# Optimization experiments

Measured on AMD Instinct MI355X. Metric: run time of the kernel, lower is better.

The kernel has to match this reference:

```python
import jax, jax.numpy as jnp
import numpy as np

EPS = 1e-6      # delta in ixaxaar/pytorch-dnc util.py and Memory.reset
CLIP = 20.0     # DNC default controller-output clip
M, Wc, R, H, IN, OUT = 10, 20, 1, 256, 27, 128
NN_IN = IN + R * Wc                 # 47 controller input size
IFACE = R * Wc + 3 * Wc + 5 * R + 3  # 88 interface vector size


def _cosine_weights(mem, keys, strengths):
    # mem (B,M,Wc), keys (B,K,Wc), strengths (B,K) -> softmax over cells of scaled cosine sim
    mem_n = mem / (jnp.linalg.norm(mem, axis=2, keepdims=True) + EPS)
    key_n = keys / (jnp.linalg.norm(keys, axis=2, keepdims=True) + EPS)
    d = jnp.einsum('bkw,bmw->bkm', key_n, mem_n)
    return jax.nn.softmax(d * strengths[:, :, None], axis=2)


def _dnc_classifier(x, W_ih, W_hh, b_ih, b_hh, W_xi, b_xi, W_fc, b_fc):
    B, T, _ = x.shape
    # ixaxaar's dnc.py builds inputs[t] = cat(x_t, last_read) ONCE with the initial
    # (zero) last_read, so read vectors never feed the next-step input.
    pad = jnp.zeros((B, R * Wc), x.dtype)
    eye_mask = 1.0 - jnp.eye(M, dtype=x.dtype)

    def step(state, x_t):
        h, c, mem, link, prec, rw, ww, usage = state
        # ---- LSTM controller (1 hidden layer, torch gate order i,f,g,o) ----
        inp = jnp.concatenate([x_t, pad], axis=1)                 # (B,47)
        gates = inp @ W_ih.T + b_ih + h @ W_hh.T + b_hh           # (B,4H)
        i, f, g, o = jnp.split(gates, 4, axis=1)
        c = jax.nn.sigmoid(f) * c + jax.nn.sigmoid(i) * jnp.tanh(g)
        h = jax.nn.sigmoid(o) * jnp.tanh(c)
        out = jnp.clip(h, -CLIP, CLIP)
        # ---- interface vector ----
        xi = out @ W_xi.T + b_xi                                  # (B,88)
        p = R * Wc
        rk = jnp.tanh(xi[:, :p]).reshape(B, R, Wc)                # read keys
        rs = jax.nn.softplus(xi[:, p:p + R]); p += R              # read strengths
        wk = jnp.tanh(xi[:, p:p + Wc]).reshape(B, 1, Wc); p += Wc # write key
        ws = jax.nn.softplus(xi[:, p:p + 1]); p += 1              # write strength
        ev = jax.nn.sigmoid(xi[:, p:p + Wc]); p += Wc             # erase vector
        wv = jnp.tanh(xi[:, p:p + Wc]); p += Wc                   # write vector
        fg = jax.nn.sigmoid(xi[:, p:p + R]); p += R               # free gates
        ag = jax.nn.sigmoid(xi[:, p:p + 1]); p += 1               # allocation gate
        wg = jax.nn.sigmoid(xi[:, p:p + 1]); p += 1               # write gate
        rm = jax.nn.softmax(xi[:, p:p + 3 * R].reshape(B, R, 3), axis=-1)  # read modes (b,f,c)
        # ---- usage (uses PREVIOUS write/read weights) ----
        usage = usage + (1 - usage) * ww
        usage = usage * jnp.prod(1 - fg[:, :, None] * rw, axis=1)
        # ---- write weighting: content + allocation (sort-based free list) ----
        cw = _cosine_weights(mem, wk, ws)[:, 0]                   # (B,M)
        u2 = EPS + (1 - EPS) * usage
        phi = jnp.argsort(u2, axis=1)
        su = jnp.take_along_axis(u2, phi, axis=1)
        prod_excl = jnp.cumprod(jnp.concatenate([jnp.ones((B, 1), u2.dtype), su], axis=1), axis=1)[:, :-1]
        alloc = jnp.take_along_axis((1 - su) * prod_excl, jnp.argsort(phi, axis=1), axis=1)
        ww = wg * (ag * alloc + (1 - ag) * cw)                    # (B,M)
        # ---- erase + write memory ----
        mem = mem * (1 - ww[:, :, None] * ev[:, None, :]) + ww[:, :, None] * wv[:, None, :]
        # ---- temporal link matrix + precedence ----
        link = (1 - ww[:, :, None] - ww[:, None, :]) * link + ww[:, :, None] * prec[:, None, :]
        link = link * eye_mask
        prec = (1 - jnp.sum(ww, axis=1, keepdims=True)) * prec + ww
        # ---- read weighting (content + forward/backward temporal) ----
        cwr = _cosine_weights(mem, rk, rs)                        # (B,R,M)
        fw = jnp.einsum('brm,bnm->brn', rw, link)                 # forward  = L @ w
        bw = jnp.einsum('brm,bmn->brn', rw, link)                 # backward = L^T @ w
        rw = rm[:, :, 0:1] * bw + rm[:, :, 1:2] * fw + rm[:, :, 2:3] * cwr
        return (h, c, mem, link, prec, rw, ww, usage), None

    z = jnp.zeros
    state0 = (z((B, H), x.dtype), z((B, H), x.dtype),
              jnp.full((B, M, Wc), EPS, x.dtype), z((B, M, M), x.dtype),
              z((B, M), x.dtype), jnp.full((B, R, M), EPS, x.dtype),
              jnp.full((B, M), EPS, x.dtype), z((B, M), x.dtype))
    (h, *_), _ = jax.lax.scan(step, state0, jnp.swapaxes(x, 0, 1))
    # classifier head: fc1 on final controller hidden state
    return h @ W_fc.T + b_fc


def setup_inputs() -> dict:
    key = jax.random.key(0)
    ks = jax.random.split(key, 10)
    B, T = 128, 512
    kb = 1.0 / np.sqrt(H)
    u = lambda kk, shape: jax.random.uniform(kk, shape, jnp.float32, -kb, kb)
    return {
        'x': jax.random.normal(ks[0], (B, T, IN), jnp.float32),
        'input_lengths': jax.random.randint(ks[1], (B,), 1, T + 1).astype(jnp.int32),
        'W_ih': u(ks[2], (4 * H, NN_IN)),
        'W_hh': u(ks[3], (4 * H, H)),
        'b_ih': u(ks[4], (4 * H,)),
        'b_hh': u(ks[5], (4 * H,)),
        'W_xi': u(ks[6], (IFACE, H)),
        'b_xi': u(ks[7], (IFACE,)),
        'W_fc': u(ks[8], (OUT, H)),
        'b_fc': u(ks[9], (OUT,)),
    }


def reference(x, input_lengths, W_ih, W_hh, b_ih, b_hh, W_xi, b_xi, W_fc, b_fc):
    # input_lengths is unpacked and discarded by DNCClassifier.forward
    return _dnc_classifier(x, W_ih, W_hh, b_ih, b_hh, W_xi, b_xi, W_fc, b_fc)
```

## Files before the change

kernel.cpp:

```cpp
#include <hip/hip_runtime.h>
#include <hip/hip_fp16.h>


typedef _Float16 h2t __attribute__((ext_vector_type(2)));
typedef unsigned int u32x4 __attribute__((ext_vector_type(4)));

#if defined(__has_builtin)
#  if __has_builtin(__builtin_amdgcn_fdot2)
#    define HAVE_FDOT2 1
#  endif
#endif

__device__ __forceinline__ h2t bc2(unsigned int v) {
  union { unsigned int u; h2t h; } x; x.u = v; return x.h;
}
__device__ __forceinline__ unsigned int pk(float a, float b) {
  union { h2t h; unsigned int u; } x;
  x.h[0] = (_Float16)a; x.h[1] = (_Float16)b;
  return x.u;
}
__device__ __forceinline__ float fdot2f(h2t a, h2t b, float c) {
#ifdef HAVE_FDOT2
  return __builtin_amdgcn_fdot2(a, b, c, false);
#else
  return c + (float)a[0] * (float)b[0] + (float)a[1] * (float)b[1];
#endif
}
__device__ __forceinline__ float dot4(u32x4 w, u32x4 h, float a) {
  a = fdot2f(bc2(w[0]), bc2(h[0]), a);
  a = fdot2f(bc2(w[1]), bc2(h[1]), a);
  a = fdot2f(bc2(w[2]), bc2(h[2]), a);
  a = fdot2f(bc2(w[3]), bc2(h[3]), a);
  return a;
}
__device__ __forceinline__ float sigmf_(float x) {
  return 1.f / (1.f + __expf(-x));
}
__device__ __forceinline__ float tanhf_(float x) {
  float xc = fminf(15.f, fmaxf(-15.f, x));
  float e = __expf(2.f * xc);
  return (e - 1.f) / (e + 1.f);
}
__device__ __forceinline__ float dpp_x1(float x) {
  return __int_as_float(
      __builtin_amdgcn_mov_dpp(__float_as_int(x), 0xB1, 0xF, 0xF, true));
}
__device__ __forceinline__ float dpp_x2(float x) {
  return __int_as_float(
      __builtin_amdgcn_mov_dpp(__float_as_int(x), 0x4E, 0xF, 0xF, true));
}

#define WS_P_OFF      0ull
#define WS_WSCAN_OFF  134217728ull
#define WS_WLDS_OFF   134643712ull
#define WS_WSTR_OFF   134725632ull
#define WS_NEED       134742016ull

__global__ void prep_w(const float* __restrict__ W_hh,
                       unsigned char* __restrict__ ws) {
  int idx = blockIdx.x * 256 + threadIdx.x;
  unsigned int* dst; int j, f;
  if (idx < 106496) {
    j = idx; dst = (unsigned int*)(ws + WS_WSCAN_OFF); f = (j >> 2) >> 9;
  } else if (idx < 126976) {
    j = idx - 106496; dst = (unsigned int*)(ws + WS_WLDS_OFF);
    f = 52 + ((j >> 2) >> 9);
  } else {
    j = idx - 126976; dst = (unsigned int*)(ws + WS_WSTR_OFF);
    f = 62 + ((j >> 2) >> 9);
  }
  int e = j & 3, vv = (j >> 2) & 511;
  int w = vv >> 6, l = vv & 63, kq = l & 3, p = l >> 2;
  int q = f >> 3, uu = (f >> 2) & 1, g = f & 3;
  int u = w * 32 + 2 * p + uu;
  int row = g * 256 + u;
  int k2 = kq * 32 + q * 4 + e;
  dst[j] = pk(W_hh[row * 256 + 2 * k2], W_hh[row * 256 + 2 * k2 + 1]);
}

__global__ __launch_bounds__(256) void prep_p(const float* __restrict__ x,
                                              const float* __restrict__ W_ih,
                                              const float* __restrict__ b_ih,
                                              const float* __restrict__ b_hh,
                                              unsigned char* __restrict__ ws) {
  __shared__ unsigned int sX[64][14];
  const int u = threadIdx.x;
  const int t = blockIdx.x >> 1;
  const int b0 = (blockIdx.x & 1) << 6;
  unsigned int wih[4][14];
  float bias[4];
#pragma unroll
  for (int g = 0; g < 4; ++g) {
    const float* row = W_ih + (size_t)(g * 256 + u) * 47;
    bias[g] = b_ih[g * 256 + u] + b_hh[g * 256 + u];
#pragma unroll
    for (int j = 0; j < 14; ++j) {
      float a = row[2 * j];
      float b = (2 * j + 1 < 27) ? row[2 * j + 1] : 0.f;
      wih[g][j] = pk(a, b);
    }
  }
#pragma unroll 1
  for (int j = u; j < 896; j += 256) {
    int row = j / 14, c2 = j - 14 * row;
    const float* xr = x + ((size_t)(b0 + row) * 512 + t) * 27;
    float a = xr[2 * c2];
    float bb = (2 * c2 + 1 < 27) ? xr[2 * c2 + 1] : 0.f;
    sX[row][c2] = pk(a, bb);
  }
  __syncthreads();
  uint2* Pout = (uint2*)(ws + WS_P_OFF);
#pragma unroll 2
  for (int p = 0; p < 64; ++p) {
    float a0 = bias[0], a1 = bias[1], a2 = bias[2], a3 = bias[3];
#pragma unroll
    for (int j = 0; j < 14; ++j) {
      h2t xx = bc2(sX[p][j]);
      a0 = fdot2f(bc2(wih[0][j]), xx, a0);
      a1 = fdot2f(bc2(wih[1][j]), xx, a1);
      a2 = fdot2f(bc2(wih[2][j]), xx, a2);
      a3 = fdot2f(bc2(wih[3][j]), xx, a3);
    }
    uint2 o; o.x = pk(a0, a1); o.y = pk(a2, a3);
    Pout[((size_t)t * 128 + (b0 + p)) * 256 + u] = o;
  }
}

__global__ __launch_bounds__(512, 2) void scan_k(
    const unsigned char* __restrict__ ws, const float* __restrict__ W_fc,
    const float* __restrict__ b_fc, float* __restrict__ out) {
  __shared__ u32x4 sWq[10 * 512];
  __shared__ __align__(16) unsigned int sH[2][160];
  __shared__ float sHF[256];
  const int v = threadIdx.x;
  const int b = blockIdx.x;
  const int l = v & 63;
  const int w = v >> 6;
  const int kq = l & 3;
  const int p = l >> 2;
  const int u_own = w * 32 + 2 * p + ((l >> 1) & 1);

  u32x4 wr[52];
  {
    const u32x4* wsc = (const u32x4*)(ws + WS_WSCAN_OFF);
#pragma unroll
    for (int f = 0; f < 52; ++f) wr[f] = wsc[f * 512 + v];
  }
  {
    const u32x4* wld = (const u32x4*)(ws + WS_WLDS_OFF);
#pragma unroll
    for (int fl = 0; fl < 10; ++fl) sWq[fl * 512 + v] = wld[fl * 512 + v];
  }
  const u32x4* wstr = (const u32x4*)(ws + WS_WSTR_OFF);

  if (v < 320) ((unsigned int*)sH)[v] = 0u;
  const uint2* Pbuf = (const uint2*)(ws + WS_P_OFF);
  const char* hbase = (const char*)sH;
  char* hwbase = (char*)sH;
  const int kqoff = kq * 144;
  float c = 0.f, hval = 0.f;
  __syncthreads();

#pragma unroll 1
  for (int t = 0; t < 512; ++t) {
    u32x4 tw0 = wstr[0 * 512 + v];
    u32x4 tw1 = wstr[1 * 512 + v];
    uint2 pP = Pbuf[((size_t)t * 128 + b) * 256 + u_own];

    const char* hb = hbase + (t & 1) * 640 + kqoff;
    float aA0 = 0.f, aA1 = 0.f, aA2 = 0.f, aA3 = 0.f;
    float aB0 = 0.f, aB1 = 0.f, aB2 = 0.f, aB3 = 0.f;
    u32x4 hq;
    hq = *(const u32x4*)(hb + 0);
    aA0 = dot4(wr[0], hq, aA0);  aA1 = dot4(wr[1], hq, aA1);
    aA2 = dot4(wr[2], hq, aA2);  aA3 = dot4(wr[3], hq, aA3);
    aB0 = dot4(wr[4], hq, aB0);  aB1 = dot4(wr[5], hq, aB1);
    aB2 = dot4(wr[6], hq, aB2);  aB3 = dot4(wr[7], hq, aB3);
    hq = *(const u32x4*)(hb + 16);
    aA0 = dot4(wr[8], hq, aA0);  aA1 = dot4(wr[9], hq, aA1);
    aA2 = dot4(wr[10], hq, aA2); aA3 = dot4(wr[11], hq, aA3);
    aB0 = dot4(wr[12], hq, aB0); aB1 = dot4(wr[13], hq, aB1);
    aB2 = dot4(wr[14], hq, aB2); aB3 = dot4(wr[15], hq, aB3);
    hq = *(const u32x4*)(hb + 32);
    aA0 = dot4(wr[16], hq, aA0); aA1 = dot4(wr[17], hq, aA1);
    aA2 = dot4(wr[18], hq, aA2); aA3 = dot4(wr[19], hq, aA3);
    aB0 = dot4(wr[20], hq, aB0); aB1 = dot4(wr[21], hq, aB1);
    aB2 = dot4(wr[22], hq, aB2); aB3 = dot4(wr[23], hq, aB3);
    hq = *(const u32x4*)(hb + 48);
    aA0 = dot4(wr[24], hq, aA0); aA1 = dot4(wr[25], hq, aA1);
    aA2 = dot4(wr[26], hq, aA2); aA3 = dot4(wr[27], hq, aA3);
    aB0 = dot4(wr[28], hq, aB0); aB1 = dot4(wr[29], hq, aB1);
    aB2 = dot4(wr[30], hq, aB2); aB3 = dot4(wr[31], hq, aB3);
    hq = *(const u32x4*)(hb + 64);
    aA0 = dot4(wr[32], hq, aA0); aA1 = dot4(wr[33], hq, aA1);
    aA2 = dot4(wr[34], hq, aA2); aA3 = dot4(wr[35], hq, aA3);
    aB0 = dot4(wr[36], hq, aB0); aB1 = dot4(wr[37], hq, aB1);
    aB2 = dot4(wr[38], hq, aB2); aB3 = dot4(wr[39], hq, aB3);
    hq = *(const u32x4*)(hb + 80);
    aA0 = dot4(wr[40], hq, aA0); aA1 = dot4(wr[41], hq, aA1);
    aA2 = dot4(wr[42], hq, aA2); aA3 = dot4(wr[43], hq, aA3);
    aB0 = dot4(wr[44], hq, aB0); aB1 = dot4(wr[45], hq, aB1);
    aB2 = dot4(wr[46], hq, aB2); aB3 = dot4(wr[47], hq, aB3);
    hq = *(const u32x4*)(hb + 96);
    aA0 = dot4(wr[48], hq, aA0); aA1 = dot4(wr[49], hq, aA1);
    aA2 = dot4(wr[50], hq, aA2); aA3 = dot4(wr[51], hq, aA3);
    aB0 = dot4(sWq[0 * 512 + v], hq, aB0); aB1 = dot4(sWq[1 * 512 + v], hq, aB1);
    aB2 = dot4(sWq[2 * 512 + v], hq, aB2); aB3 = dot4(sWq[3 * 512 + v], hq, aB3);
    hq = *(const u32x4*)(hb + 112);
    aA0 = dot4(sWq[4 * 512 + v], hq, aA0); aA1 = dot4(sWq[5 * 512 + v], hq, aA1);
    aA2 = dot4(sWq[6 * 512 + v], hq, aA2); aA3 = dot4(sWq[7 * 512 + v], hq, aA3);
    aB0 = dot4(sWq[8 * 512 + v], hq, aB0); aB1 = dot4(sWq[9 * 512 + v], hq, aB1);
    aB2 = dot4(tw0, hq, aB2); aB3 = dot4(tw1, hq, aB3);

    aA0 += dpp_x1(aA0); aA0 += dpp_x2(aA0);
    aA1 += dpp_x1(aA1); aA1 += dpp_x2(aA1);
    aA2 += dpp_x1(aA2); aA2 += dpp_x2(aA2);
    aA3 += dpp_x1(aA3); aA3 += dpp_x2(aA3);
    aB0 += dpp_x1(aB0); aB0 += dpp_x2(aB0);
    aB1 += dpp_x1(aB1); aB1 += dpp_x2(aB1);
    aB2 += dpp_x1(aB2); aB2 += dpp_x2(aB2);
    aB3 += dpp_x1(aB3); aB3 += dpp_x2(aB3);

    float gi = (l & 2) ? aB0 : aA0;
    float gf = (l & 2) ? aB1 : aA1;
    float gg = (l & 2) ? aB2 : aA2;
    float go = (l & 2) ? aB3 : aA3;
    h2t p01 = bc2(pP.x), p23 = bc2(pP.y);
    gi += (float)p01[0]; gf += (float)p01[1];
    gg += (float)p23[0]; go += (float)p23[1];
    c = sigmf_(gf) * c + sigmf_(gi) * tanhf_(gg);
    hval = sigmf_(go) * tanhf_(c);
    if (!(l & 1)) {
      _Float16* hw = (_Float16*)(hwbase + ((t + 1) & 1) * 640);
      hw[u_own + (u_own >> 6) * 8] = (_Float16)hval;
    }
    __syncthreads();
  }

  if (!(l & 1)) sHF[u_own] = hval;
  __syncthreads();
  if (v < 128) {
    const float4* wrow = (const float4*)(W_fc + (size_t)v * 256);
    float a = b_fc[v];
#pragma unroll 8
    for (int q = 0; q < 64; ++q) {
      float4 wq = wrow[q];
      float4 hh = ((const float4*)sHF)[q];
      a += wq.x * hh.x + wq.y * hh.y + wq.z * hh.z + wq.w * hh.w;
    }
    out[(size_t)b * 128 + v] = a;
  }
}

extern "C" void kernel_launch(void* const* d_in, const int* in_sizes, int n_in,
                              void* d_out, int out_size, void* d_ws,
                              size_t ws_size, hipStream_t stream) {
  const float* x    = (const float*)d_in[0];
  const float* W_ih = (const float*)d_in[2];
  const float* W_hh = (const float*)d_in[3];
  const float* b_ih = (const float*)d_in[4];
  const float* b_hh = (const float*)d_in[5];
  const float* W_fc = (const float*)d_in[8];
  const float* b_fc = (const float*)d_in[9];
  unsigned char* ws = (unsigned char*)d_ws;

  if (ws_size < WS_NEED) return;

  prep_w<<<512, 256, 0, stream>>>(W_hh, ws);
  prep_p<<<1024, 256, 0, stream>>>(x, W_ih, b_ih, b_hh, ws);
  scan_k<<<128, 512, 0, stream>>>(ws, W_fc, b_fc, (float*)d_out);
}
```

Baseline: 917.9 us.

## Double scan block to 1024 threads, one hidden unit per 4-lane group

Reorganizes the recurrent scan so each 1024-thread block gives every hidden unit its own 4-lane group computing all four gates, instead of 512 threads each doing two units' worth of gate dot products. Per-thread register weights drop from 52 to 24 vectors, and the remaining 8 slices go to LDS, which removes the per-step global weight stream loads. The aim is to halve the serial per-step dot-product chain and the select logic. In exchange, each block-wide barrier now synchronizes 16 waves, and only one block of 1024 threads can fit per CU.

```diff
diff --git a/kernel.cpp b/kernel.cpp
--- a/kernel.cpp
+++ b/kernel.cpp
@@ -50,32 +50,22 @@
       __builtin_amdgcn_mov_dpp(__float_as_int(x), 0x4E, 0xF, 0xF, true));
 }
 
-#define WS_P_OFF      0ull
-#define WS_WSCAN_OFF  134217728ull
-#define WS_WLDS_OFF   134643712ull
-#define WS_WSTR_OFF   134725632ull
-#define WS_NEED       134742016ull
+#define WS_P_OFF   0ull
+#define WS_W_OFF   134217728ull
+#define WS_NEED    134742016ull
 
 __global__ void prep_w(const float* __restrict__ W_hh,
                        unsigned char* __restrict__ ws) {
   int idx = blockIdx.x * 256 + threadIdx.x;
-  unsigned int* dst; int j, f;
-  if (idx < 106496) {
-    j = idx; dst = (unsigned int*)(ws + WS_WSCAN_OFF); f = (j >> 2) >> 9;
-  } else if (idx < 126976) {
-    j = idx - 106496; dst = (unsigned int*)(ws + WS_WLDS_OFF);
-    f = 52 + ((j >> 2) >> 9);
-  } else {
-    j = idx - 126976; dst = (unsigned int*)(ws + WS_WSTR_OFF);
-    f = 62 + ((j >> 2) >> 9);
-  }
-  int e = j & 3, vv = (j >> 2) & 511;
-  int w = vv >> 6, l = vv & 63, kq = l & 3, p = l >> 2;
-  int q = f >> 3, uu = (f >> 2) & 1, g = f & 3;
-  int u = w * 32 + 2 * p + uu;
+  int f = idx >> 12, rem = idx & 4095;
+  int v = rem >> 2, e = rem & 3;
+  int w = v >> 6, l = v & 63, kq = l & 3, pl = l >> 2;
+  int u = w * 16 + pl;
+  int j = f >> 2, g = f & 3;
   int row = g * 256 + u;
-  int k2 = kq * 32 + q * 4 + e;
-  dst[j] = pk(W_hh[row * 256 + 2 * k2], W_hh[row * 256 + 2 * k2 + 1]);
+  int k2 = kq * 32 + j * 4 + e;
+  ((unsigned int*)(ws + WS_W_OFF))[idx] =
+      pk(W_hh[row * 256 + 2 * k2], W_hh[row * 256 + 2 * k2 + 1]);
 }
 
 __global__ __launch_bounds__(256) void prep_p(const float* __restrict__ x,
@@ -126,10 +116,10 @@
   }
 }
 
-__global__ __launch_bounds__(512, 2) void scan_k(
+__global__ __launch_bounds__(1024) void scan_k(
     const unsigned char* __restrict__ ws, const float* __restrict__ W_fc,
     const float* __restrict__ b_fc, float* __restrict__ out) {
-  __shared__ u32x4 sWq[10 * 512];
+  __shared__ u32x4 sWq[8 * 1024];
   __shared__ __align__(16) unsigned int sH[2][160];
   __shared__ float sHF[256];
   const int v = threadIdx.x;
@@ -137,107 +127,79 @@
   const int l = v & 63;
   const int w = v >> 6;
   const int kq = l & 3;
-  const int p = l >> 2;
-  const int u_own = w * 32 + 2 * p + ((l >> 1) & 1);
-
-  u32x4 wr[52];
-  {
-    const u32x4* wsc = (const u32x4*)(ws + WS_WSCAN_OFF);
-#pragma unroll
-    for (int f = 0; f < 52; ++f) wr[f] = wsc[f * 512 + v];
-  }
-  {
-    const u32x4* wld = (const u32x4*)(ws + WS_WLDS_OFF);
-#pragma unroll
-    for (int fl = 0; fl < 10; ++fl) sWq[fl * 512 + v] = wld[fl * 512 + v];
-  }
-  const u32x4* wstr = (const u32x4*)(ws + WS_WSTR_OFF);
+  const int pl = l >> 2;
+  const int u = w * 16 + pl;
+
+  const u32x4* Wall = (const u32x4*)(ws + WS_W_OFF);
+  u32x4 wr[24];
+#pragma unroll
+  for (int f = 0; f < 24; ++f) wr[f] = Wall[f * 1024 + v];
+#pragma unroll
+  for (int f = 0; f < 8; ++f) sWq[f * 1024 + v] = Wall[(24 + f) * 1024 + v];
 
   if (v < 320) ((unsigned int*)sH)[v] = 0u;
   const uint2* Pbuf = (const uint2*)(ws + WS_P_OFF);
   const char* hbase = (const char*)sH;
-  char* hwbase = (char*)sH;
   const int kqoff = kq * 144;
+  const int hwb = (u >> 6) * 144 + ((u & 63) >> 1) * 4 + (u & 1) * 2;
   float c = 0.f, hval = 0.f;
   __syncthreads();
 
 #pragma unroll 1
   for (int t = 0; t < 512; ++t) {
-    u32x4 tw0 = wstr[0 * 512 + v];
-    u32x4 tw1 = wstr[1 * 512 + v];
-    uint2 pP = Pbuf[((size_t)t * 128 + b) * 256 + u_own];
+    uint2 pP = Pbuf[((size_t)t * 128 + b) * 256 + u];
 
     const char* hb = hbase + (t & 1) * 640 + kqoff;
-    float aA0 = 0.f, aA1 = 0.f, aA2 = 0.f, aA3 = 0.f;
-    float aB0 = 0.f, aB1 = 0.f, aB2 = 0.f, aB3 = 0.f;
+    float a0 = 0.f, a1 = 0.f, a2 = 0.f, a3 = 0.f;
     u32x4 hq;
     hq = *(const u32x4*)(hb + 0);
-    aA0 = dot4(wr[0], hq, aA0);  aA1 = dot4(wr[1], hq, aA1);
-    aA2 = dot4(wr[2], hq, aA2);  aA3 = dot4(wr[3], hq, aA3);
-    aB0 = dot4(wr[4], hq, aB0);  aB1 = dot4(wr[5], hq, aB1);
-    aB2 = dot4(wr[6], hq, aB2);  aB3 = dot4(wr[7], hq, aB3);
+    a0 = dot4(wr[0], hq, a0);  a1 = dot4(wr[1], hq, a1);
+    a2 = dot4(wr[2], hq, a2);  a3 = dot4(wr[3], hq, a3);
     hq = *(const u32x4*)(hb + 16);
-    aA0 = dot4(wr[8], hq, aA0);  aA1 = dot4(wr[9], hq, aA1);
-    aA2 = dot4(wr[10], hq, aA2); aA3 = dot4(wr[11], hq, aA3);
-    aB0 = dot4(wr[12], hq, aB0); aB1 = dot4(wr[13], hq, aB1);
-    aB2 = dot4(wr[14], hq, aB2); aB3 = dot4(wr[15], hq, aB3);
+    a0 = dot4(wr[4], hq, a0);  a1 = dot4(wr[5], hq, a1);
+    a2 = dot4(wr[6], hq, a2);  a3 = dot4(wr[7], hq, a3);
     hq = *(const u32x4*)(hb + 32);
-    aA0 = dot4(wr[16], hq, aA0); aA1 = dot4(wr[17], hq, aA1);
-    aA2 = dot4(wr[18], hq, aA2); aA3 = dot4(wr[19], hq, aA3);
-    aB0 = dot4(wr[20], hq, aB0); aB1 = dot4(wr[21], hq, aB1);
-    aB2 = dot4(wr[22], hq, aB2); aB3 = dot4(wr[23], hq, aB3);
+    a0 = dot4(wr[8], hq, a0);  a1 = dot4(wr[9], hq, a1);
+    a2 = dot4(wr[10], hq, a2); a3 = dot4(wr[11], hq, a3);
     hq = *(const u32x4*)(hb + 48);
-    aA0 = dot4(wr[24], hq, aA0); aA1 = dot4(wr[25], hq, aA1);
-    aA2 = dot4(wr[26], hq, aA2); aA3 = dot4(wr[27], hq, aA3);
-    aB0 = dot4(wr[28], hq, aB0); aB1 = dot4(wr[29], hq, aB1);
-    aB2 = dot4(wr[30], hq, aB2); aB3 = dot4(wr[31], hq, aB3);
+    a0 = dot4(wr[12], hq, a0); a1 = dot4(wr[13], hq, a1);
+    a2 = dot4(wr[14], hq, a2); a3 = dot4(wr[15], hq, a3);
     hq = *(const u32x4*)(hb + 64);
-    aA0 = dot4(wr[32], hq, aA0); aA1 = dot4(wr[33], hq, aA1);
-    aA2 = dot4(wr[34], hq, aA2); aA3 = dot4(wr[35], hq, aA3);
-    aB0 = dot4(wr[36], hq, aB0); aB1 = dot4(wr[37], hq, aB1);
-    aB2 = dot4(wr[38], hq, aB2); aB3 = dot4(wr[39], hq, aB3);
+    a0 = dot4(wr[16], hq, a0); a1 = dot4(wr[17], hq, a1);
+    a2 = dot4(wr[18], hq, a2); a3 = dot4(wr[19], hq, a3);
     hq = *(const u32x4*)(hb + 80);
-    aA0 = dot4(wr[40], hq, aA0); aA1 = dot4(wr[41], hq, aA1);
-    aA2 = dot4(wr[42], hq, aA2); aA3 = dot4(wr[43], hq, aA3);
-    aB0 = dot4(wr[44], hq, aB0); aB1 = dot4(wr[45], hq, aB1);
-    aB2 = dot4(wr[46], hq, aB2); aB3 = dot4(wr[47], hq, aB3);
+    a0 = dot4(wr[20], hq, a0); a1 = dot4(wr[21], hq, a1);
+    a2 = dot4(wr[22], hq, a2); a3 = dot4(wr[23], hq, a3);
     hq = *(const u32x4*)(hb + 96);
-    aA0 = dot4(wr[48], hq, aA0); aA1 = dot4(wr[49], hq, aA1);
-    aA2 = dot4(wr[50], hq, aA2); aA3 = dot4(wr[51], hq, aA3);
-    aB0 = dot4(sWq[0 * 512 + v], hq, aB0); aB1 = dot4(sWq[1 * 512 + v], hq, aB1);
-    aB2 = dot4(sWq[2 * 512 + v], hq, aB2); aB3 = dot4(sWq[3 * 512 + v], hq, aB3);
+    a0 = dot4(sWq[0 * 1024 + v], hq, a0);
+    a1 = dot4(sWq[1 * 1024 + v], hq, a1);
+    a2 = dot4(sWq[2 * 1024 + v], hq, a2);
+    a3 = dot4(sWq[3 * 1024 + v], hq, a3);
     hq = *(const u32x4*)(hb + 112);
-    aA0 = dot4(sWq[4 * 512 + v], hq, aA0); aA1 = dot4(sWq[5 * 512 + v], hq, aA1);
-    aA2 = dot4(sWq[6 * 512 + v], hq, aA2); aA3 = dot4(sWq[7 * 512 + v], hq, aA3);
-    aB0 = dot4(sWq[8 * 512 + v], hq, aB0); aB1 = dot4(sWq[9 * 512 + v], hq, aB1);
-    aB2 = dot4(tw0, hq, aB2); aB3 = dot4(tw1, hq, aB3);
-
-    aA0 += dpp_x1(aA0); aA0 += dpp_x2(aA0);
-    aA1 += dpp_x1(aA1); aA1 += dpp_x2(aA1);
-    aA2 += dpp_x1(aA2); aA2 += dpp_x2(aA2);
-    aA3 += dpp_x1(aA3); aA3 += dpp_x2(aA3);
-    aB0 += dpp_x1(aB0); aB0 += dpp_x2(aB0);
-    aB1 += dpp_x1(aB1); aB1 += dpp_x2(aB1);
-    aB2 += dpp_x1(aB2); aB2 += dpp_x2(aB2);
-    aB3 += dpp_x1(aB3); aB3 += dpp_x2(aB3);
-
-    float gi = (l & 2) ? aB0 : aA0;
-    float gf = (l & 2) ? aB1 : aA1;
-    float gg = (l & 2) ? aB2 : aA2;
-    float go = (l & 2) ? aB3 : aA3;
+    a0 = dot4(sWq[4 * 1024 + v], hq, a0);
+    a1 = dot4(sWq[5 * 1024 + v], hq, a1);
+    a2 = dot4(sWq[6 * 1024 + v], hq, a2);
+    a3 = dot4(sWq[7 * 1024 + v], hq, a3);
+
+    a0 += dpp_x1(a0); a0 += dpp_x2(a0);
+    a1 += dpp_x1(a1); a1 += dpp_x2(a1);
+    a2 += dpp_x1(a2); a2 += dpp_x2(a2);
+    a3 += dpp_x1(a3); a3 += dpp_x2(a3);
+
     h2t p01 = bc2(pP.x), p23 = bc2(pP.y);
-    gi += (float)p01[0]; gf += (float)p01[1];
-    gg += (float)p23[0]; go += (float)p23[1];
+    float gi = a0 + (float)p01[0];
+    float gf = a1 + (float)p01[1];
+    float gg = a2 + (float)p23[0];
+    float go = a3 + (float)p23[1];
     c = sigmf_(gf) * c + sigmf_(gi) * tanhf_(gg);
     hval = sigmf_(go) * tanhf_(c);
-    if (!(l & 1)) {
-      _Float16* hw = (_Float16*)(hwbase + ((t + 1) & 1) * 640);
-      hw[u_own + (u_own >> 6) * 8] = (_Float16)hval;
+    if (kq == 0) {
+      *(_Float16*)((char*)sH + ((t + 1) & 1) * 640 + hwb) = (_Float16)hval;
     }
     __syncthreads();
   }
 
-  if (!(l & 1)) sHF[u_own] = hval;
+  if (kq == 0) sHF[u] = hval;
   __syncthreads();
   if (v < 128) {
     const float4* wrow = (const float4*)(W_fc + (size_t)v * 256);
@@ -268,5 +230,5 @@
 
   prep_w<<<512, 256, 0, stream>>>(W_hh, ws);
   prep_p<<<1024, 256, 0, stream>>>(x, W_ih, b_ih, b_hh, ws);
-  scan_k<<<128, 512, 0, stream>>>(ws, W_fc, b_fc, (float*)d_out);
-}
+  scan_k<<<128, 1024, 0, stream>>>(ws, W_fc, b_fc, (float*)d_out);
+}
```

Measured after the change: 1.258 ms. 37.0% more time.

## Move streamed weight slices to LDS, prefetch next-step inputs, use fast reciprocal activations

Applied to the files above, without the earlier changes.

The last two weight fragments were previously re-read from global memory on every timestep. They are now staged once into LDS, which grows from 10 to 12 slices per thread. The precomputed input projection for the next timestep is loaded one iteration ahead to hide global latency, and the loop is unrolled by two. Sigmoid and tanh now use the hardware reciprocal, and tanh drops its clamp; the clamp removal relies on exp overflowing to inf and giving the correct limit. The larger LDS footprint may hurt the two-blocks-per-CU occupancy target.

```diff
diff --git a/kernel.cpp b/kernel.cpp
--- a/kernel.cpp
+++ b/kernel.cpp
@@ -34,12 +34,13 @@
   return a;
 }
 __device__ __forceinline__ float sigmf_(float x) {
-  return 1.f / (1.f + __expf(-x));
+  float e = __expf(-x);
+  return __builtin_amdgcn_rcpf(1.f + e);
 }
 __device__ __forceinline__ float tanhf_(float x) {
-  float xc = fminf(15.f, fmaxf(-15.f, x));
-  float e = __expf(2.f * xc);
-  return (e - 1.f) / (e + 1.f);
+  float e = __expf(2.f * x);
+  float r = __builtin_amdgcn_rcpf(1.f + e);
+  return __builtin_fmaf(-2.f, r, 1.f);
 }
 __device__ __forceinline__ float dpp_x1(float x) {
   return __int_as_float(
@@ -53,29 +54,26 @@
 #define WS_P_OFF      0ull
 #define WS_WSCAN_OFF  134217728ull
 #define WS_WLDS_OFF   134643712ull
-#define WS_WSTR_OFF   134725632ull
 #define WS_NEED       134742016ull
 
 __global__ void prep_w(const float* __restrict__ W_hh,
                        unsigned char* __restrict__ ws) {
   int idx = blockIdx.x * 256 + threadIdx.x;
-  unsigned int* dst; int j, f;
+  unsigned int* dst; int j4, f;
   if (idx < 106496) {
-    j = idx; dst = (unsigned int*)(ws + WS_WSCAN_OFF); f = (j >> 2) >> 9;
-  } else if (idx < 126976) {
-    j = idx - 106496; dst = (unsigned int*)(ws + WS_WLDS_OFF);
-    f = 52 + ((j >> 2) >> 9);
+    j4 = idx; dst = (unsigned int*)(ws + WS_WSCAN_OFF);
+    f = (j4 >> 2) >> 9;
   } else {
-    j = idx - 126976; dst = (unsigned int*)(ws + WS_WSTR_OFF);
-    f = 62 + ((j >> 2) >> 9);
-  }
-  int e = j & 3, vv = (j >> 2) & 511;
+    j4 = idx - 106496; dst = (unsigned int*)(ws + WS_WLDS_OFF);
+    f = 52 + ((j4 >> 2) >> 9);
+  }
+  int e = j4 & 3, vv = (j4 >> 2) & 511;
   int w = vv >> 6, l = vv & 63, kq = l & 3, p = l >> 2;
-  int q = f >> 3, uu = (f >> 2) & 1, g = f & 3;
+  int j = f >> 3, uu = (f >> 2) & 1, g = f & 3;
   int u = w * 32 + 2 * p + uu;
   int row = g * 256 + u;
-  int k2 = kq * 32 + q * 4 + e;
-  dst[j] = pk(W_hh[row * 256 + 2 * k2], W_hh[row * 256 + 2 * k2 + 1]);
+  int k2 = kq * 32 + j * 4 + e;
+  dst[j4] = pk(W_hh[row * 256 + 2 * k2], W_hh[row * 256 + 2 * k2 + 1]);
 }
 
 __global__ __launch_bounds__(256) void prep_p(const float* __restrict__ x,
@@ -129,7 +127,7 @@
 __global__ __launch_bounds__(512, 2) void scan_k(
     const unsigned char* __restrict__ ws, const float* __restrict__ W_fc,
     const float* __restrict__ b_fc, float* __restrict__ out) {
-  __shared__ u32x4 sWq[10 * 512];
+  __shared__ u32x4 sWq[12 * 512];
   __shared__ __align__(16) unsigned int sH[2][160];
   __shared__ float sHF[256];
   const int v = threadIdx.x;
@@ -149,23 +147,21 @@
   {
     const u32x4* wld = (const u32x4*)(ws + WS_WLDS_OFF);
 #pragma unroll
-    for (int fl = 0; fl < 10; ++fl) sWq[fl * 512 + v] = wld[fl * 512 + v];
-  }
-  const u32x4* wstr = (const u32x4*)(ws + WS_WSTR_OFF);
+    for (int fl = 0; fl < 12; ++fl) sWq[fl * 512 + v] = wld[fl * 512 + v];
+  }
 
   if (v < 320) ((unsigned int*)sH)[v] = 0u;
   const uint2* Pbuf = (const uint2*)(ws + WS_P_OFF);
   const char* hbase = (const char*)sH;
-  char* hwbase = (char*)sH;
   const int kqoff = kq * 144;
   float c = 0.f, hval = 0.f;
+  uint2 pP = Pbuf[(size_t)b * 256 + u_own];
   __syncthreads();
 
-#pragma unroll 1
+#pragma unroll 2
   for (int t = 0; t < 512; ++t) {
-    u32x4 tw0 = wstr[0 * 512 + v];
-    u32x4 tw1 = wstr[1 * 512 + v];
-    uint2 pP = Pbuf[((size_t)t * 128 + b) * 256 + u_own];
+    int tn = (t + 1) & 511;
+    uint2 pPn = Pbuf[((size_t)tn * 128 + b) * 256 + u_own];
 
     const char* hb = hbase + (t & 1) * 640 + kqoff;
     float aA0 = 0.f, aA1 = 0.f, aA2 = 0.f, aA3 = 0.f;
@@ -204,13 +200,19 @@
     hq = *(const u32x4*)(hb + 96);
     aA0 = dot4(wr[48], hq, aA0); aA1 = dot4(wr[49], hq, aA1);
     aA2 = dot4(wr[50], hq, aA2); aA3 = dot4(wr[51], hq, aA3);
-    aB0 = dot4(sWq[0 * 512 + v], hq, aB0); aB1 = dot4(sWq[1 * 512 + v], hq, aB1);
-    aB2 = dot4(sWq[2 * 512 + v], hq, aB2); aB3 = dot4(sWq[3 * 512 + v], hq, aB3);
+    aB0 = dot4(sWq[0 * 512 + v], hq, aB0);
+    aB1 = dot4(sWq[1 * 512 + v], hq, aB1);
+    aB2 = dot4(sWq[2 * 512 + v], hq, aB2);
+    aB3 = dot4(sWq[3 * 512 + v], hq, aB3);
     hq = *(const u32x4*)(hb + 112);
-    aA0 = dot4(sWq[4 * 512 + v], hq, aA0); aA1 = dot4(sWq[5 * 512 + v], hq, aA1);
-    aA2 = dot4(sWq[6 * 512 + v], hq, aA2); aA3 = dot4(sWq[7 * 512 + v], hq, aA3);
-    aB0 = dot4(sWq[8 * 512 + v], hq, aB0); aB1 = dot4(sWq[9 * 512 + v], hq, aB1);
-    aB2 = dot4(tw0, hq, aB2); aB3 = dot4(tw1, hq, aB3);
+    aA0 = dot4(sWq[4 * 512 + v], hq, aA0);
+    aA1 = dot4(sWq[5 * 512 + v], hq, aA1);
+    aA2 = dot4(sWq[6 * 512 + v], hq, aA2);
+    aA3 = dot4(sWq[7 * 512 + v], hq, aA3);
+    aB0 = dot4(sWq[8 * 512 + v], hq, aB0);
+    aB1 = dot4(sWq[9 * 512 + v], hq, aB1);
+    aB2 = dot4(sWq[10 * 512 + v], hq, aB2);
+    aB3 = dot4(sWq[11 * 512 + v], hq, aB3);
 
     aA0 += dpp_x1(aA0); aA0 += dpp_x2(aA0);
     aA1 += dpp_x1(aA1); aA1 += dpp_x2(aA1);
@@ -231,9 +233,10 @@
     c = sigmf_(gf) * c + sigmf_(gi) * tanhf_(gg);
     hval = sigmf_(go) * tanhf_(c);
     if (!(l & 1)) {
-      _Float16* hw = (_Float16*)(hwbase + ((t + 1) & 1) * 640);
+      _Float16* hw = (_Float16*)((char*)sH + ((t + 1) & 1) * 640);
       hw[u_own + (u_own >> 6) * 8] = (_Float16)hval;
     }
+    pP = pPn;
     __syncthreads();
   }
 
```

New measurement: 945.6 us. 3.0% more time.
